# Optimization experiments

Hardware: AMD Instinct MI355X
Metric: run time of the kernel (lower is better)

The kernel has to match this reference:

```python
import jax, jax.numpy as jnp
import numpy as np

B, N, C, M, OUT = 4, 256, 32, 4, 64


def _uniform(k, shape, fan_in):
    s = 1.0 / np.sqrt(fan_in)
    return jax.random.uniform(k, shape, jnp.float32, -s, s)


def setup_inputs() -> dict:
    key = jax.random.key(0)
    ks = jax.random.split(key, 11)
    return {
        "x": jax.random.normal(ks[0], (B, N, N, C), jnp.float32),
        # Neighborhood / SnConv2to1 linears (in=C, out=M neighborhood channels)
        "w1_nb": _uniform(ks[1], (3 * C, M), 3 * C),
        "b1_nb": _uniform(ks[2], (M,), 3 * C),
        "w0_nb": _uniform(ks[3], (2 * C, M), 2 * C),
        "b0_nb": _uniform(ks[4], (M,), 2 * C),
        # SnConv2 linears (in channels = M*C after neighborhood product)
        "w2d": _uniform(ks[5], (2 * M * C, OUT), 2 * M * C),
        "b2d": _uniform(ks[6], (OUT,), 2 * M * C),
        "w1d": _uniform(ks[7], (3 * M * C, OUT), 3 * M * C),
        "b1d": _uniform(ks[8], (OUT,), 3 * M * C),
        "w0d": _uniform(ks[9], (2 * M * C, OUT), 2 * M * C),
        "b0d": _uniform(ks[10], (OUT,), 2 * M * C),
    }


def _contractions(x):
    # x: [B, n, n, c]; mask=None, reduction='mean' path of _get_contractions
    n = x.shape[1]
    rowsum = x.sum(axis=1) / n                      # [B, n, c]
    colsum = x.sum(axis=2) / n                      # [B, n, c]
    diag = jnp.diagonal(x, axis1=1, axis2=2)        # [B, c, n]
    rowcolsum = x.sum(axis=(1, 2)) / (n * n)        # [B, c]
    diag_sum = diag.sum(axis=-1) / n                # [B, c]  (/= sqrt(n^2))
    diag = jnp.moveaxis(diag, -1, 1)                # move_from_end -> [B, n, c]
    return rowsum, colsum, diag, rowcolsum, diag_sum


def reference(x, w1_nb, b1_nb, w0_nb, b0_nb, w2d, b2d, w1d, b1d, w0d, b0d):
    # ---- Neighborhood: SnConv2to1 -> sigmoid ----
    rs, cs, dg, rcs, ds = _contractions(x)
    obj1 = jnp.concatenate([rs, cs, dg], axis=-1)             # [B, n, 3C]
    obj0 = jnp.concatenate([rcs, ds], axis=-1)                # [B, 2C]
    node = obj1 @ w1_nb + b1_nb + (obj0 @ w0_nb + b0_nb)[:, None, :]
    neighbs = jax.nn.sigmoid(node)                            # [B, n, M]
    # ---- _neighbor_elementwise_product ----
    expanded = neighbs[:, None, :, :] * neighbs[:, :, None, :]  # [B, n, n, M]
    # channel_product: outer product over channel dims, collapsed to M*C
    xl = (expanded[..., :, None] * x[..., None, :]).reshape(B, N, N, M * C)
    # ---- SnConv2 on the localized tensor ----
    rs2, cs2, dg2, rcs2, ds2 = _contractions(xl)
    obj2d = jnp.concatenate([xl, jnp.swapaxes(xl, 1, 2)], axis=-1)  # [B,n,n,2MC]
    obj1d = jnp.concatenate([rs2, cs2, dg2], axis=-1)               # [B,n,3MC]
    obj0d = jnp.concatenate([rcs2, ds2], axis=-1)                   # [B,2MC]
    out = (obj2d @ w2d + b2d
           + (obj1d @ w1d + b1d)[:, None, :, :]
           + (obj0d @ w0d + b0d)[:, None, None, :])                 # [B,n,n,OUT]
    return out
```

## Files before the change

kernel.cpp:

```cpp
#include <hip/hip_runtime.h>
#include <math.h>

#define Bv 4
#define Nv 256
#define Cv 32
#define Mv 4
#define OUTv 64
#define MCv (Mv*Cv)

typedef _Float16 h8 __attribute__((ext_vector_type(8)));
typedef _Float16 h4 __attribute__((ext_vector_type(4)));
typedef float f4 __attribute__((ext_vector_type(4)));

__device__ __align__(16) float g_xT  [Bv * Nv * Nv * Cv];
__device__ __align__(16) float g_rs  [Bv * Nv * Cv];
__device__ __align__(16) float g_cs  [Bv * Nv * Cv];
__device__ __align__(16) float g_dgx [Bv * Nv * Cv];
__device__ __align__(16) float g_nb  [Bv * Nv * Mv];
__device__ __align__(16) float g_rcs2R[8 * Bv * MCv];
__device__ __align__(16) float g_ds2R [8 * Bv * MCv];
__device__ __align__(16) float g_addv[Bv * Nv * OUTv];
__device__ __align__(16) _Float16 g_wfrag[8 * 4 * 64 * 8];

__global__ __launch_bounds__(256) void k_transpose(const float* __restrict__ x) {
    int it = blockIdx.x, jt = blockIdx.y, b = blockIdx.z;
    int i0 = it * 8, j0 = jt * 32;
    int t = threadIdx.x;
    __shared__ __align__(16) float4 T[32 * 65];
    const float4* x4  = (const float4*)(x    + (size_t)b * Nv * Nv * Cv);
    float4*       xT4 = (float4*)      (g_xT + (size_t)b * Nv * Nv * Cv);
    #pragma unroll
    for (int r = 0; r < 8; r++) {
        int j = t >> 3, c4 = t & 7;
        T[j * 65 + r * 8 + c4] = x4[((size_t)(i0 + r) * Nv + j0 + j) * 8 + c4];
    }
    __syncthreads();
    #pragma unroll
    for (int r = 0; r < 8; r++) {
        int idx = r * 256 + t;
        int j = idx >> 6, i = (idx >> 3) & 7, c4 = idx & 7;
        xT4[((size_t)(j0 + j) * Nv + i0 + i) * 8 + c4] = T[j * 65 + i * 8 + c4];
    }
}

__global__ __launch_bounds__(256) void k_contract1(const float* __restrict__ x,
                                                   const float* __restrict__ w2d) {
    int bx = blockIdx.x, b = blockIdx.y;
    int t = threadIdx.x;
    if (bx >= 2 * Nv) {
        if (b != 0) return;
        int r = bx - 2 * Nv;
        if (r == 8) {
            float4 z = {0.f,0.f,0.f,0.f};
            #pragma unroll
            for (int k = 0; k < 4; k++) {
                ((float4*)g_rcs2R)[k * 256 + t] = z;
                ((float4*)g_ds2R )[k * 256 + t] = z;
            }
            return;
        }
        int fi = r * 256 + t;
        int s = fi >> 8, q = (fi >> 6) & 3, lane = fi & 63;
        int k0 = s * 32 + ((lane >> 4) << 3);
        int o = q * 16 + (lane & 15);
        #pragma unroll
        for (int jj = 0; jj < 8; jj++)
            g_wfrag[fi * 8 + jj] = (_Float16)w2d[(size_t)(k0 + jj) * OUTv + o];
        return;
    }
    int c4 = t & 7, sub = t >> 3;
    __shared__ float red[32][36];
    float4 acc = {0.f,0.f,0.f,0.f};
    if (bx < Nv) {
        int n = bx;
        const float4* xT4 = (const float4*)(g_xT + (size_t)b * Nv * Nv * Cv);
        for (int i = sub; i < Nv; i += 32) {
            float4 v = xT4[((size_t)n * Nv + i) * 8 + c4];
            acc.x += v.x; acc.y += v.y; acc.z += v.z; acc.w += v.w;
        }
        red[sub][c4*4+0] = acc.x; red[sub][c4*4+1] = acc.y;
        red[sub][c4*4+2] = acc.z; red[sub][c4*4+3] = acc.w;
        __syncthreads();
        if (t < 32) {
            float s = 0.f;
            #pragma unroll
            for (int k = 0; k < 32; k++) s += red[k][t];
            g_rs[(b * Nv + n) * Cv + t] = s * (1.0f / Nv);
        }
        if (t < 8) {
            const float4* xb4 = (const float4*)(x + (size_t)b * Nv * Nv * Cv);
            ((float4*)g_dgx)[(b * Nv + n) * 8 + t] = xb4[((size_t)n * Nv + n) * 8 + t];
        }
    } else {
        int n = bx - Nv;
        const float4* xb4 = (const float4*)(x + (size_t)b * Nv * Nv * Cv);
        for (int j = sub; j < Nv; j += 32) {
            float4 v = xb4[((size_t)n * Nv + j) * 8 + c4];
            acc.x += v.x; acc.y += v.y; acc.z += v.z; acc.w += v.w;
        }
        red[sub][c4*4+0] = acc.x; red[sub][c4*4+1] = acc.y;
        red[sub][c4*4+2] = acc.z; red[sub][c4*4+3] = acc.w;
        __syncthreads();
        if (t < 32) {
            float s = 0.f;
            #pragma unroll
            for (int k = 0; k < 32; k++) s += red[k][t];
            g_cs[(b * Nv + n) * Cv + t] = s * (1.0f / Nv);
        }
    }
}

__global__ __launch_bounds__(256) void k_fused(const float* __restrict__ x,
    const float* __restrict__ w1, const float* __restrict__ b1,
    const float* __restrict__ w0, const float* __restrict__ b0,
    const float* __restrict__ w1d, const float* __restrict__ b1d,
    const float* __restrict__ b2d, const float* __restrict__ b0d) {
    int n = blockIdx.x, b = blockIdx.y;
    int t = threadIdx.x;

    __shared__ float red8[8][64];
    __shared__ float obj0[64];
    __shared__ float t0nb[4];
    __shared__ __align__(16) float nb4[Nv][4];
    __shared__ float red[32][132];
    __shared__ float S1l[MCv], S2l[MCv];
    __shared__ float redD[4][64];

    {
        int c = t & 31, sub = t >> 5;
        float ar = 0.f, ad = 0.f;
        for (int nn = sub; nn < Nv; nn += 8) {
            ar += g_rs[(b * Nv + nn) * Cv + c];
            ad += g_dgx[(b * Nv + nn) * Cv + c];
        }
        red8[sub][c] = ar;
        red8[sub][32 + c] = ad;
    }
    __syncthreads();
    if (t < 64) {
        float s = 0.f;
        #pragma unroll
        for (int k = 0; k < 8; k++) s += red8[k][t];
        obj0[t] = s * (1.0f / Nv);
    }
    __syncthreads();
    if (t < 4) {
        float v = b0[t];
        for (int k = 0; k < 2 * Cv; k++) v += obj0[k] * w0[k * Mv + t];
        t0nb[t] = v;
    }
    __syncthreads();
    {
        const float4* rs4 = (const float4*)(g_rs  + (size_t)(b * Nv + t) * Cv);
        const float4* cs4 = (const float4*)(g_cs  + (size_t)(b * Nv + t) * Cv);
        const float4* dg4 = (const float4*)(g_dgx + (size_t)(b * Nv + t) * Cv);
        float node[4];
        #pragma unroll
        for (int m = 0; m < 4; m++) node[m] = t0nb[m] + b1[m];
        #pragma unroll
        for (int q = 0; q < 8; q++) {
            float4 R = rs4[q], S = cs4[q], D = dg4[q];
            #pragma unroll
            for (int e = 0; e < 4; e++) {
                int cc = q * 4 + e;
                float r = ((const float*)&R)[e];
                float s = ((const float*)&S)[e];
                float d = ((const float*)&D)[e];
                #pragma unroll
                for (int m = 0; m < 4; m++)
                    node[m] += r * w1[cc * Mv + m] + s * w1[(Cv + cc) * Mv + m]
                             + d * w1[(2 * Cv + cc) * Mv + m];
            }
        }
        float4 nv;
        #pragma unroll
        for (int m = 0; m < 4; m++)
            ((float*)&nv)[m] = 1.0f / (1.0f + expf(-node[m]));
        *(float4*)nb4[t] = nv;
        if (n == 0) ((float4*)g_nb)[b * Nv + t] = nv;
    }
    __syncthreads();

    const float4* xb4  = (const float4*)(x    + (size_t)b * Nv * Nv * Cv);
    const float4* xT4b = (const float4*)(g_xT + (size_t)b * Nv * Nv * Cv);
    int c4 = t & 7, sub3 = t >> 3;

    {
        float4 a[4];
        #pragma unroll
        for (int m = 0; m < 4; m++) a[m] = {0.f,0.f,0.f,0.f};
        for (int i = sub3; i < Nv; i += 32) {
            float4 v = xT4b[((size_t)n * Nv + i) * 8 + c4];
            float4 nv = *(const float4*)nb4[i];
            a[0].x += nv.x*v.x; a[0].y += nv.x*v.y; a[0].z += nv.x*v.z; a[0].w += nv.x*v.w;
            a[1].x += nv.y*v.x; a[1].y += nv.y*v.y; a[1].z += nv.y*v.z; a[1].w += nv.y*v.w;
            a[2].x += nv.z*v.x; a[2].y += nv.z*v.y; a[2].z += nv.z*v.z; a[2].w += nv.z*v.w;
            a[3].x += nv.w*v.x; a[3].y += nv.w*v.y; a[3].z += nv.w*v.z; a[3].w += nv.w*v.w;
        }
        #pragma unroll
        for (int m = 0; m < 4; m++) {
            red[sub3][m*32 + c4*4+0] = a[m].x; red[sub3][m*32 + c4*4+1] = a[m].y;
            red[sub3][m*32 + c4*4+2] = a[m].z; red[sub3][m*32 + c4*4+3] = a[m].w;
        }
    }
    __syncthreads();
    if (t < 128) {
        float s = 0.f;
        #pragma unroll
        for (int k = 0; k < 32; k++) s += red[k][t];
        S1l[t] = s;
        int m = t >> 5, c = t & 31;
        float nv = nb4[n][m];
        int rep = ((n & 7) * Bv + b) * MCv + t;
        atomicAdd(&g_rcs2R[rep], nv * s);
        atomicAdd(&g_ds2R [rep], nv * nv * g_dgx[(b * Nv + n) * Cv + c]);
    }
    __syncthreads();

    {
        float4 a[4];
        #pragma unroll
        for (int m = 0; m < 4; m++) a[m] = {0.f,0.f,0.f,0.f};
        for (int j = sub3; j < Nv; j += 32) {
            float4 v = xb4[((size_t)n * Nv + j) * 8 + c4];
            float4 nv = *(const float4*)nb4[j];
            a[0].x += nv.x*v.x; a[0].y += nv.x*v.y; a[0].z += nv.x*v.z; a[0].w += nv.x*v.w;
            a[1].x += nv.y*v.x; a[1].y += nv.y*v.y; a[1].z += nv.y*v.z; a[1].w += nv.y*v.w;
            a[2].x += nv.z*v.x; a[2].y += nv.z*v.y; a[2].z += nv.z*v.z; a[2].w += nv.z*v.w;
            a[3].x += nv.w*v.x; a[3].y += nv.w*v.y; a[3].z += nv.w*v.z; a[3].w += nv.w*v.w;
        }
        #pragma unroll
        for (int m = 0; m < 4; m++) {
            red[sub3][m*32 + c4*4+0] = a[m].x; red[sub3][m*32 + c4*4+1] = a[m].y;
            red[sub3][m*32 + c4*4+2] = a[m].z; red[sub3][m*32 + c4*4+3] = a[m].w;
        }
    }
    __syncthreads();
    if (t < 128) {
        float s = 0.f;
        #pragma unroll
        for (int k = 0; k < 32; k++) s += red[k][t];
        S2l[t] = s;
    }
    __syncthreads();

    {
        int o = t & 63, ks = t >> 6;
        const float invN = 1.0f / Nv;
        float nv = nb4[n][ks];
        float f = nv * invN, d2 = nv * nv;
        const float* dgr = g_dgx + (size_t)(b * Nv + n) * Cv;
        float acc = 0.f;
        #pragma unroll 8
        for (int cc = 0; cc < 32; cc++) {
            int mc = ks * 32 + cc;
            acc += f * S1l[mc] * w1d[(size_t)mc * OUTv + o]
                 + f * S2l[mc] * w1d[(size_t)(MCv + mc) * OUTv + o]
                 + d2 * dgr[cc] * w1d[(size_t)(2 * MCv + mc) * OUTv + o];
        }
        redD[ks][o] = acc;
    }
    __syncthreads();
    if (t < 64) {
        float v = redD[0][t] + redD[1][t] + redD[2][t] + redD[3][t]
                + b1d[t] + b2d[t] + b0d[t];
        g_addv[(size_t)(b * Nv + n) * OUTv + t] = v;
    }
}

#define XPAD 40
__global__ __launch_bounds__(256) void k_main(const float* __restrict__ x,
                                              float* __restrict__ out,
                                              const float* __restrict__ w0d) {
    int jt = blockIdx.x, ip = blockIdx.y, b = blockIdx.z;
    int i0 = ip * 2, i1 = i0 + 1;
    int j0 = jt * 128;
    int t = threadIdx.x;
    int lane = t & 63, w = t >> 6;
    int rowA = lane & 15, quad = lane >> 4;

    __shared__ __align__(16) _Float16 Wl[8 * 4 * 64 * 8];
    __shared__ __align__(16) _Float16 Xt0[128 * XPAD];
    __shared__ __align__(16) _Float16 Xb0[128 * XPAD];
    __shared__ __align__(16) _Float16 Xt1[128 * XPAD];
    __shared__ __align__(16) _Float16 Xb1[128 * XPAD];
    __shared__ float rcl[MCv], dsl[MCv];
    __shared__ float t0red[4][64];
    __shared__ float t0l[64];

    {
        const float4* src = (const float4*)g_wfrag;
        float4* dst = (float4*)Wl;
        #pragma unroll
        for (int r = 0; r < 8; r++) dst[r * 256 + t] = src[r * 256 + t];
    }
    {
        const float4* x4  = (const float4*)x;
        const float4* xT4 = (const float4*)g_xT;
        #pragma unroll
        for (int r = 0; r < 4; r++) {
            int idx = r * 256 + t;
            int j = idx >> 3, c4 = idx & 7;
            float4 v0 = x4 [((size_t)(b * Nv + i0) * Nv + j0 + j) * 8 + c4];
            float4 v1 = x4 [((size_t)(b * Nv + i1) * Nv + j0 + j) * 8 + c4];
            float4 u0 = xT4[((size_t)(b * Nv + i0) * Nv + j0 + j) * 8 + c4];
            float4 u1 = xT4[((size_t)(b * Nv + i1) * Nv + j0 + j) * 8 + c4];
            h4 h0; h0[0] = (_Float16)v0.x; h0[1] = (_Float16)v0.y;
            h0[2] = (_Float16)v0.z; h0[3] = (_Float16)v0.w;
            *(h4*)&Xt0[j * XPAD + c4 * 4] = h0;
            h4 h1; h1[0] = (_Float16)v1.x; h1[1] = (_Float16)v1.y;
            h1[2] = (_Float16)v1.z; h1[3] = (_Float16)v1.w;
            *(h4*)&Xt1[j * XPAD + c4 * 4] = h1;
            h4 g0; g0[0] = (_Float16)u0.x; g0[1] = (_Float16)u0.y;
            g0[2] = (_Float16)u0.z; g0[3] = (_Float16)u0.w;
            *(h4*)&Xb0[j * XPAD + c4 * 4] = g0;
            h4 g1; g1[0] = (_Float16)u1.x; g1[1] = (_Float16)u1.y;
            g1[2] = (_Float16)u1.z; g1[3] = (_Float16)u1.w;
            *(h4*)&Xb1[j * XPAD + c4 * 4] = g1;
        }
    }
    if (t < 128) {
        float s = 0.f;
        #pragma unroll
        for (int r = 0; r < 8; r++) s += g_rcs2R[(r * Bv + b) * MCv + t];
        rcl[t] = s;
    } else {
        int tt = t - 128;
        float s = 0.f;
        #pragma unroll
        for (int r = 0; r < 8; r++) s += g_ds2R[(r * Bv + b) * MCv + tt];
        dsl[tt] = s;
    }
    int jl1 = w * 32 + rowA, jl2 = jl1 + 16;
    _Float16 e1h0[4], e2h0[4], e1h1[4], e2h1[4];
    {
        const float* ni0 = g_nb + (size_t)(b * Nv + i0) * Mv;
        const float* ni1 = g_nb + (size_t)(b * Nv + i1) * Mv;
        const float* n1 = g_nb + (size_t)(b * Nv + j0 + jl1) * Mv;
        const float* n2 = g_nb + (size_t)(b * Nv + j0 + jl2) * Mv;
        #pragma unroll
        for (int m = 0; m < 4; m++) {
            e1h0[m] = (_Float16)(ni0[m] * n1[m]);
            e2h0[m] = (_Float16)(ni0[m] * n2[m]);
            e1h1[m] = (_Float16)(ni1[m] * n1[m]);
            e2h1[m] = (_Float16)(ni1[m] * n2[m]);
        }
    }
    __syncthreads();
    {
        int o = t & 63, ks = t >> 6;
        const float invN = 1.0f / Nv;
        const float invN2 = invN * invN;
        float a0 = 0.f;
        #pragma unroll 8
        for (int cc = 0; cc < 32; cc++) {
            int mc = ks * 32 + cc;
            a0 += invN2 * rcl[mc] * w0d[(size_t)mc * OUTv + o]
                + invN  * dsl[mc] * w0d[(size_t)(MCv + mc) * OUTv + o];
        }
        t0red[ks][o] = a0;
    }
    __syncthreads();
    if (t < 64) t0l[t] = t0red[0][t] + t0red[1][t] + t0red[2][t] + t0red[3][t];
    __syncthreads();

    f4 acc[2][2][4];
    #pragma unroll
    for (int ii = 0; ii < 2; ii++)
        #pragma unroll
        for (int js = 0; js < 2; js++)
            #pragma unroll
            for (int q = 0; q < 4; q++) acc[ii][js][q] = {0.f, 0.f, 0.f, 0.f};

    const h8* Wf = (const h8*)Wl;
    #pragma unroll
    for (int part = 0; part < 2; part++) {
        const _Float16* X0 = part ? Xb0 : Xt0;
        const _Float16* X1 = part ? Xb1 : Xt1;
        h8 xv1_0 = *(const h8*)&X0[jl1 * XPAD + quad * 8];
        h8 xv2_0 = *(const h8*)&X0[jl2 * XPAD + quad * 8];
        h8 xv1_1 = *(const h8*)&X1[jl1 * XPAD + quad * 8];
        h8 xv2_1 = *(const h8*)&X1[jl2 * XPAD + quad * 8];
        #pragma unroll
        for (int m = 0; m < 4; m++) {
            h8 a1_0 = xv1_0 * e1h0[m];
            h8 a2_0 = xv2_0 * e2h0[m];
            h8 a1_1 = xv1_1 * e1h1[m];
            h8 a2_1 = xv2_1 * e2h1[m];
            int s = part * 4 + m;
            #pragma unroll
            for (int q = 0; q < 4; q++) {
                h8 bf = Wf[(s * 4 + q) * 64 + lane];
                acc[0][0][q] = __builtin_amdgcn_mfma_f32_16x16x32_f16(a1_0, bf, acc[0][0][q], 0, 0, 0);
                acc[0][1][q] = __builtin_amdgcn_mfma_f32_16x16x32_f16(a2_0, bf, acc[0][1][q], 0, 0, 0);
                acc[1][0][q] = __builtin_amdgcn_mfma_f32_16x16x32_f16(a1_1, bf, acc[1][0][q], 0, 0, 0);
                acc[1][1][q] = __builtin_amdgcn_mfma_f32_16x16x32_f16(a2_1, bf, acc[1][1][q], 0, 0, 0);
            }
        }
    }
    #pragma unroll
    for (int js = 0; js < 2; js++) {
        int jbase = j0 + w * 32 + js * 16 + quad * 4;
        #pragma unroll
        for (int q = 0; q < 4; q++) {
            int o = q * 16 + rowA;
            float tv = t0l[o];
            #pragma unroll
            for (int r = 0; r < 4; r++) {
                int j = jbase + r;
                float av = g_addv[(size_t)(b * Nv + j) * OUTv + o] + tv;
                out[(((size_t)(b * Nv + i0)) * Nv + j) * OUTv + o] = acc[0][js][q][r] + av;
                out[(((size_t)(b * Nv + i1)) * Nv + j) * OUTv + o] = acc[1][js][q][r] + av;
            }
        }
    }
}

extern "C" void kernel_launch(void* const* d_in, const int* in_sizes, int n_in,
                              void* d_out, int out_size, void* d_ws, size_t ws_size,
                              hipStream_t stream) {
    const float* x     = (const float*)d_in[0];
    const float* w1_nb = (const float*)d_in[1];
    const float* b1_nb = (const float*)d_in[2];
    const float* w0_nb = (const float*)d_in[3];
    const float* b0_nb = (const float*)d_in[4];
    const float* w2d   = (const float*)d_in[5];
    const float* b2d   = (const float*)d_in[6];
    const float* w1d   = (const float*)d_in[7];
    const float* b1d   = (const float*)d_in[8];
    const float* w0d   = (const float*)d_in[9];
    const float* b0d   = (const float*)d_in[10];
    float* out = (float*)d_out;
    (void)d_ws; (void)ws_size;

    hipLaunchKernelGGL(k_transpose, dim3(Nv / 8, Nv / 32, Bv), dim3(256), 0, stream, x);
    hipLaunchKernelGGL(k_contract1, dim3(2 * Nv + 9, Bv), dim3(256), 0, stream, x, w2d);
    hipLaunchKernelGGL(k_fused, dim3(Nv, Bv), dim3(256), 0, stream,
                       x, w1_nb, b1_nb, w0_nb, b0_nb, w1d, b1d, b2d, b0d);
    hipLaunchKernelGGL(k_main, dim3(2, Nv / 2, Bv), dim3(256), 0, stream, x, out, w0d);
}
```

Before: 182.1 us.

## Fuse colsum partials into transpose, hoist neighborhood into own kernel, overlap row/col passes

The transpose kernel now also produces partial column sums from its shared tile, so k_contract1 no longer re-reads x for colsums and only launches half as many reduction blocks. The neighborhood sigmoid computation, which every k_fused block used to repeat, moves into a separate small k_neighb kernel that writes g_nb once. k_fused then runs the transposed and original reductions concurrently in two halves of the block instead of two serial passes. The cost is an extra launch and a tiny 4-block kernel on the critical path, plus a partial-sum buffer.

```diff
diff --git a/kernel.cpp b/kernel.cpp
--- a/kernel.cpp
+++ b/kernel.cpp
@@ -13,6 +13,7 @@
 typedef float f4 __attribute__((ext_vector_type(4)));
 
 __device__ __align__(16) float g_xT  [Bv * Nv * Nv * Cv];
+__device__ __align__(16) float g_csP [8 * Bv * Nv * Cv];
 __device__ __align__(16) float g_rs  [Bv * Nv * Cv];
 __device__ __align__(16) float g_cs  [Bv * Nv * Cv];
 __device__ __align__(16) float g_dgx [Bv * Nv * Cv];
@@ -41,15 +42,23 @@
         int j = idx >> 6, i = (idx >> 3) & 7, c4 = idx & 7;
         xT4[((size_t)(j0 + j) * Nv + i0 + i) * 8 + c4] = T[j * 65 + i * 8 + c4];
     }
+    {
+        int r = t >> 5, c = t & 31;
+        const float* Tf = (const float*)T;
+        float s = 0.f;
+        #pragma unroll
+        for (int j = 0; j < 32; j++) s += Tf[j * 260 + r * 32 + c];
+        g_csP[((size_t)jt * Bv + b) * Nv * Cv + (i0 + r) * Cv + c] = s;
+    }
 }
 
 __global__ __launch_bounds__(256) void k_contract1(const float* __restrict__ x,
                                                    const float* __restrict__ w2d) {
     int bx = blockIdx.x, b = blockIdx.y;
     int t = threadIdx.x;
-    if (bx >= 2 * Nv) {
+    if (bx >= Nv) {
         if (b != 0) return;
-        int r = bx - 2 * Nv;
+        int r = bx - Nv;
         if (r == 8) {
             float4 z = {0.f,0.f,0.f,0.f};
             #pragma unroll
@@ -71,183 +80,142 @@
     int c4 = t & 7, sub = t >> 3;
     __shared__ float red[32][36];
     float4 acc = {0.f,0.f,0.f,0.f};
-    if (bx < Nv) {
-        int n = bx;
-        const float4* xT4 = (const float4*)(g_xT + (size_t)b * Nv * Nv * Cv);
-        for (int i = sub; i < Nv; i += 32) {
-            float4 v = xT4[((size_t)n * Nv + i) * 8 + c4];
-            acc.x += v.x; acc.y += v.y; acc.z += v.z; acc.w += v.w;
-        }
-        red[sub][c4*4+0] = acc.x; red[sub][c4*4+1] = acc.y;
-        red[sub][c4*4+2] = acc.z; red[sub][c4*4+3] = acc.w;
-        __syncthreads();
-        if (t < 32) {
-            float s = 0.f;
-            #pragma unroll
-            for (int k = 0; k < 32; k++) s += red[k][t];
-            g_rs[(b * Nv + n) * Cv + t] = s * (1.0f / Nv);
-        }
-        if (t < 8) {
-            const float4* xb4 = (const float4*)(x + (size_t)b * Nv * Nv * Cv);
-            ((float4*)g_dgx)[(b * Nv + n) * 8 + t] = xb4[((size_t)n * Nv + n) * 8 + t];
-        }
-    } else {
-        int n = bx - Nv;
+    int n = bx;
+    const float4* xT4 = (const float4*)(g_xT + (size_t)b * Nv * Nv * Cv);
+    for (int i = sub; i < Nv; i += 32) {
+        float4 v = xT4[((size_t)n * Nv + i) * 8 + c4];
+        acc.x += v.x; acc.y += v.y; acc.z += v.z; acc.w += v.w;
+    }
+    red[sub][c4*4+0] = acc.x; red[sub][c4*4+1] = acc.y;
+    red[sub][c4*4+2] = acc.z; red[sub][c4*4+3] = acc.w;
+    __syncthreads();
+    if (t < 32) {
+        float s = 0.f;
+        #pragma unroll
+        for (int k = 0; k < 32; k++) s += red[k][t];
+        g_rs[(b * Nv + n) * Cv + t] = s * (1.0f / Nv);
+        float csv = 0.f;
+        #pragma unroll
+        for (int p = 0; p < 8; p++)
+            csv += g_csP[((size_t)p * Bv + b) * Nv * Cv + n * Cv + t];
+        g_cs[(b * Nv + n) * Cv + t] = csv * (1.0f / Nv);
+    }
+    if (t < 8) {
         const float4* xb4 = (const float4*)(x + (size_t)b * Nv * Nv * Cv);
-        for (int j = sub; j < Nv; j += 32) {
-            float4 v = xb4[((size_t)n * Nv + j) * 8 + c4];
-            acc.x += v.x; acc.y += v.y; acc.z += v.z; acc.w += v.w;
-        }
-        red[sub][c4*4+0] = acc.x; red[sub][c4*4+1] = acc.y;
-        red[sub][c4*4+2] = acc.z; red[sub][c4*4+3] = acc.w;
-        __syncthreads();
-        if (t < 32) {
-            float s = 0.f;
-            #pragma unroll
-            for (int k = 0; k < 32; k++) s += red[k][t];
-            g_cs[(b * Nv + n) * Cv + t] = s * (1.0f / Nv);
-        }
-    }
+        ((float4*)g_dgx)[(b * Nv + n) * 8 + t] = xb4[((size_t)n * Nv + n) * 8 + t];
+    }
+}
+
+__global__ void k_neighb(const float* __restrict__ w1, const float* __restrict__ b1,
+                         const float* __restrict__ w0, const float* __restrict__ b0) {
+    int b = blockIdx.x, t = threadIdx.x;
+    int c = t & 31, sub = t >> 5;
+    float ar = 0.f, ad = 0.f;
+    for (int n = sub; n < Nv; n += 8) {
+        ar += g_rs[(b * Nv + n) * Cv + c];
+        ad += g_dgx[(b * Nv + n) * Cv + c];
+    }
+    __shared__ float red[8][64];
+    __shared__ float obj0[64];
+    __shared__ float redm[64][4];
+    __shared__ float t0nb[4];
+    red[sub][c] = ar;
+    red[sub][32 + c] = ad;
+    __syncthreads();
+    if (t < 64) {
+        float s = 0.f;
+        #pragma unroll
+        for (int k = 0; k < 8; k++) s += red[k][t];
+        obj0[t] = s * (1.0f / Nv);
+    }
+    __syncthreads();
+    {
+        int k = t >> 2, m = t & 3;
+        redm[k][m] = obj0[k] * w0[k * Mv + m];
+    }
+    __syncthreads();
+    if (t < 4) {
+        float v = b0[t];
+        #pragma unroll
+        for (int k = 0; k < 64; k++) v += redm[k][t];
+        t0nb[t] = v;
+    }
+    __syncthreads();
+    int n = t;
+    float node[4];
+    #pragma unroll
+    for (int m = 0; m < 4; m++) node[m] = t0nb[m] + b1[m];
+    for (int cc = 0; cc < Cv; cc++) {
+        float r = g_rs[(b * Nv + n) * Cv + cc];
+        float s = g_cs[(b * Nv + n) * Cv + cc];
+        float d = g_dgx[(b * Nv + n) * Cv + cc];
+        #pragma unroll
+        for (int m = 0; m < 4; m++)
+            node[m] += r * w1[cc * Mv + m] + s * w1[(Cv + cc) * Mv + m] + d * w1[(2 * Cv + cc) * Mv + m];
+    }
+    #pragma unroll
+    for (int m = 0; m < 4; m++)
+        g_nb[(b * Nv + n) * Mv + m] = 1.0f / (1.0f + expf(-node[m]));
 }
 
 __global__ __launch_bounds__(256) void k_fused(const float* __restrict__ x,
-    const float* __restrict__ w1, const float* __restrict__ b1,
-    const float* __restrict__ w0, const float* __restrict__ b0,
     const float* __restrict__ w1d, const float* __restrict__ b1d,
     const float* __restrict__ b2d, const float* __restrict__ b0d) {
     int n = blockIdx.x, b = blockIdx.y;
     int t = threadIdx.x;
 
-    __shared__ float red8[8][64];
-    __shared__ float obj0[64];
-    __shared__ float t0nb[4];
-    __shared__ __align__(16) float nb4[Nv][4];
-    __shared__ float red[32][132];
+    __shared__ __align__(16) float4 nb4[Nv];
+    __shared__ float red[2][16][132];
     __shared__ float S1l[MCv], S2l[MCv];
     __shared__ float redD[4][64];
 
-    {
-        int c = t & 31, sub = t >> 5;
-        float ar = 0.f, ad = 0.f;
-        for (int nn = sub; nn < Nv; nn += 8) {
-            ar += g_rs[(b * Nv + nn) * Cv + c];
-            ad += g_dgx[(b * Nv + nn) * Cv + c];
-        }
-        red8[sub][c] = ar;
-        red8[sub][32 + c] = ad;
-    }
-    __syncthreads();
-    if (t < 64) {
-        float s = 0.f;
-        #pragma unroll
-        for (int k = 0; k < 8; k++) s += red8[k][t];
-        obj0[t] = s * (1.0f / Nv);
-    }
-    __syncthreads();
-    if (t < 4) {
-        float v = b0[t];
-        for (int k = 0; k < 2 * Cv; k++) v += obj0[k] * w0[k * Mv + t];
-        t0nb[t] = v;
-    }
-    __syncthreads();
-    {
-        const float4* rs4 = (const float4*)(g_rs  + (size_t)(b * Nv + t) * Cv);
-        const float4* cs4 = (const float4*)(g_cs  + (size_t)(b * Nv + t) * Cv);
-        const float4* dg4 = (const float4*)(g_dgx + (size_t)(b * Nv + t) * Cv);
-        float node[4];
-        #pragma unroll
-        for (int m = 0; m < 4; m++) node[m] = t0nb[m] + b1[m];
-        #pragma unroll
-        for (int q = 0; q < 8; q++) {
-            float4 R = rs4[q], S = cs4[q], D = dg4[q];
-            #pragma unroll
-            for (int e = 0; e < 4; e++) {
-                int cc = q * 4 + e;
-                float r = ((const float*)&R)[e];
-                float s = ((const float*)&S)[e];
-                float d = ((const float*)&D)[e];
-                #pragma unroll
-                for (int m = 0; m < 4; m++)
-                    node[m] += r * w1[cc * Mv + m] + s * w1[(Cv + cc) * Mv + m]
-                             + d * w1[(2 * Cv + cc) * Mv + m];
-            }
-        }
-        float4 nv;
-        #pragma unroll
-        for (int m = 0; m < 4; m++)
-            ((float*)&nv)[m] = 1.0f / (1.0f + expf(-node[m]));
-        *(float4*)nb4[t] = nv;
-        if (n == 0) ((float4*)g_nb)[b * Nv + t] = nv;
-    }
-    __syncthreads();
-
-    const float4* xb4  = (const float4*)(x    + (size_t)b * Nv * Nv * Cv);
-    const float4* xT4b = (const float4*)(g_xT + (size_t)b * Nv * Nv * Cv);
-    int c4 = t & 7, sub3 = t >> 3;
-
-    {
-        float4 a[4];
-        #pragma unroll
-        for (int m = 0; m < 4; m++) a[m] = {0.f,0.f,0.f,0.f};
-        for (int i = sub3; i < Nv; i += 32) {
-            float4 v = xT4b[((size_t)n * Nv + i) * 8 + c4];
-            float4 nv = *(const float4*)nb4[i];
-            a[0].x += nv.x*v.x; a[0].y += nv.x*v.y; a[0].z += nv.x*v.z; a[0].w += nv.x*v.w;
-            a[1].x += nv.y*v.x; a[1].y += nv.y*v.y; a[1].z += nv.y*v.z; a[1].w += nv.y*v.w;
-            a[2].x += nv.z*v.x; a[2].y += nv.z*v.y; a[2].z += nv.z*v.z; a[2].w += nv.z*v.w;
-            a[3].x += nv.w*v.x; a[3].y += nv.w*v.y; a[3].z += nv.w*v.z; a[3].w += nv.w*v.w;
-        }
-        #pragma unroll
-        for (int m = 0; m < 4; m++) {
-            red[sub3][m*32 + c4*4+0] = a[m].x; red[sub3][m*32 + c4*4+1] = a[m].y;
-            red[sub3][m*32 + c4*4+2] = a[m].z; red[sub3][m*32 + c4*4+3] = a[m].w;
-        }
+    nb4[t] = ((const float4*)g_nb)[b * Nv + t];
+    __syncthreads();
+
+    int half = t >> 7, tt = t & 127, c4 = tt & 7, sub = tt >> 3;
+    const float4* src4 = half
+        ? (const float4*)(x    + (size_t)b * Nv * Nv * Cv) + (size_t)n * Nv * 8
+        : (const float4*)(g_xT + (size_t)b * Nv * Nv * Cv) + (size_t)n * Nv * 8;
+    float4 a[4];
+    #pragma unroll
+    for (int m = 0; m < 4; m++) a[m] = {0.f,0.f,0.f,0.f};
+    for (int i = sub; i < Nv; i += 16) {
+        float4 v = src4[i * 8 + c4];
+        float4 nv = nb4[i];
+        a[0].x += nv.x*v.x; a[0].y += nv.x*v.y; a[0].z += nv.x*v.z; a[0].w += nv.x*v.w;
+        a[1].x += nv.y*v.x; a[1].y += nv.y*v.y; a[1].z += nv.y*v.z; a[1].w += nv.y*v.w;
+        a[2].x += nv.z*v.x; a[2].y += nv.z*v.y; a[2].z += nv.z*v.z; a[2].w += nv.z*v.w;
+        a[3].x += nv.w*v.x; a[3].y += nv.w*v.y; a[3].z += nv.w*v.z; a[3].w += nv.w*v.w;
+    }
+    #pragma unroll
+    for (int m = 0; m < 4; m++) {
+        red[half][sub][m*32 + c4*4+0] = a[m].x; red[half][sub][m*32 + c4*4+1] = a[m].y;
+        red[half][sub][m*32 + c4*4+2] = a[m].z; red[half][sub][m*32 + c4*4+3] = a[m].w;
     }
     __syncthreads();
     if (t < 128) {
         float s = 0.f;
         #pragma unroll
-        for (int k = 0; k < 32; k++) s += red[k][t];
+        for (int k = 0; k < 16; k++) s += red[0][k][t];
         S1l[t] = s;
         int m = t >> 5, c = t & 31;
-        float nv = nb4[n][m];
+        float nv = ((const float*)&nb4[n])[m];
         int rep = ((n & 7) * Bv + b) * MCv + t;
         atomicAdd(&g_rcs2R[rep], nv * s);
         atomicAdd(&g_ds2R [rep], nv * nv * g_dgx[(b * Nv + n) * Cv + c]);
-    }
-    __syncthreads();
-
-    {
-        float4 a[4];
-        #pragma unroll
-        for (int m = 0; m < 4; m++) a[m] = {0.f,0.f,0.f,0.f};
-        for (int j = sub3; j < Nv; j += 32) {
-            float4 v = xb4[((size_t)n * Nv + j) * 8 + c4];
-            float4 nv = *(const float4*)nb4[j];
-            a[0].x += nv.x*v.x; a[0].y += nv.x*v.y; a[0].z += nv.x*v.z; a[0].w += nv.x*v.w;
-            a[1].x += nv.y*v.x; a[1].y += nv.y*v.y; a[1].z += nv.y*v.z; a[1].w += nv.y*v.w;
-            a[2].x += nv.z*v.x; a[2].y += nv.z*v.y; a[2].z += nv.z*v.z; a[2].w += nv.z*v.w;
-            a[3].x += nv.w*v.x; a[3].y += nv.w*v.y; a[3].z += nv.w*v.z; a[3].w += nv.w*v.w;
-        }
-        #pragma unroll
-        for (int m = 0; m < 4; m++) {
-            red[sub3][m*32 + c4*4+0] = a[m].x; red[sub3][m*32 + c4*4+1] = a[m].y;
-            red[sub3][m*32 + c4*4+2] = a[m].z; red[sub3][m*32 + c4*4+3] = a[m].w;
-        }
-    }
-    __syncthreads();
-    if (t < 128) {
-        float s = 0.f;
-        #pragma unroll
-        for (int k = 0; k < 32; k++) s += red[k][t];
-        S2l[t] = s;
+    } else {
+        int u = t - 128;
+        float s = 0.f;
+        #pragma unroll
+        for (int k = 0; k < 16; k++) s += red[1][k][u];
+        S2l[u] = s;
     }
     __syncthreads();
 
     {
         int o = t & 63, ks = t >> 6;
         const float invN = 1.0f / Nv;
-        float nv = nb4[n][ks];
+        float nv = ((const float*)&nb4[n])[ks];
         float f = nv * invN, d2 = nv * nv;
         const float* dgr = g_dgx + (size_t)(b * Nv + n) * Cv;
         float acc = 0.f;
@@ -434,8 +402,10 @@
     (void)d_ws; (void)ws_size;
 
     hipLaunchKernelGGL(k_transpose, dim3(Nv / 8, Nv / 32, Bv), dim3(256), 0, stream, x);
-    hipLaunchKernelGGL(k_contract1, dim3(2 * Nv + 9, Bv), dim3(256), 0, stream, x, w2d);
+    hipLaunchKernelGGL(k_contract1, dim3(Nv + 9, Bv), dim3(256), 0, stream, x, w2d);
+    hipLaunchKernelGGL(k_neighb, dim3(Bv), dim3(256), 0, stream,
+                       w1_nb, b1_nb, w0_nb, b0_nb);
     hipLaunchKernelGGL(k_fused, dim3(Nv, Bv), dim3(256), 0, stream,
-                       x, w1_nb, b1_nb, w0_nb, b0_nb, w1d, b1d, b2d, b0d);
+                       x, w1d, b1d, b2d, b0d);
     hipLaunchKernelGGL(k_main, dim3(2, Nv / 2, Bv), dim3(256), 0, stream, x, out, w0d);
 }
```

Measured after the change: 177.2 us. 1.03x faster.
